# Kernel optimization log

Hardware: AMD Instinct MI355X
Metric: run time of the kernel (lower is better)

## Reference

```python
import jax, jax.numpy as jnp
import numpy as np

N_SRC, N_MID, N_TGT = 200000, 100000, 50000
E1, E2 = 1600000, 800000
D_IN, D_HID, D_OUT = 128, 256, 64


def setup_inputs() -> dict:
    key = jax.random.key(0)
    ks = jax.random.split(key, 10)
    x = jax.random.normal(ks[0], (N_SRC, D_IN), dtype=jnp.float32)
    # edge_index[0] = source node ids, edge_index[1] = target node ids (PyG source_to_target)
    ei1 = jnp.stack([
        jax.random.randint(ks[1], (E1,), 0, N_SRC, dtype=jnp.int32),
        jax.random.randint(ks[2], (E1,), 0, N_MID, dtype=jnp.int32),
    ])
    ei2 = jnp.stack([
        jax.random.randint(ks[3], (E2,), 0, N_MID, dtype=jnp.int32),
        jax.random.randint(ks[4], (E2,), 0, N_TGT, dtype=jnp.int32),
    ])
    s = 1.0 / np.sqrt(D_IN)
    Wl1 = jax.random.uniform(ks[5], (D_IN, D_HID), jnp.float32, -s, s)
    Wr1 = jax.random.uniform(ks[6], (D_IN, D_HID), jnp.float32, -s, s)
    b1 = jnp.zeros((D_HID,), jnp.float32)
    s2 = 1.0 / np.sqrt(D_HID)
    Wl2 = jax.random.uniform(ks[7], (D_HID, D_OUT), jnp.float32, -s2, s2)
    Wr2 = jax.random.uniform(ks[8], (D_HID, D_OUT), jnp.float32, -s2, s2)
    b2 = jnp.zeros((D_OUT,), jnp.float32)
    return {"x": x, "edge_index1": ei1, "edge_index2": ei2,
            "Wl1": Wl1, "Wr1": Wr1, "b1": b1,
            "Wl2": Wl2, "Wr2": Wr2, "b2": b2}


def _sage_conv(x_src, x_tgt, edge_index, Wl, Wr, b, n_tgt):
    # mean aggregation of source features onto targets, then two linear branches
    msg = x_src[edge_index[0]]                                   # [E, d]
    agg = jax.ops.segment_sum(msg, edge_index[1], num_segments=n_tgt)
    cnt = jax.ops.segment_sum(jnp.ones((edge_index.shape[1],), x_src.dtype),
                              edge_index[1], num_segments=n_tgt)
    agg = agg / jnp.maximum(cnt, 1.0)[:, None]
    return agg @ Wl + x_tgt @ Wr + b


def reference(x, edge_index1, edge_index2, Wl1, Wr1, b1, Wl2, Wr2, b2):
    # layer 1: [N_SRC, D_IN] -> [N_MID, D_HID], then ReLU (dropout inactive in eval)
    h = _sage_conv(x, x[:N_MID], edge_index1, Wl1, Wr1, b1, N_MID)
    h = jax.nn.relu(h)
    # layer 2 (final): no activation
    out = _sage_conv(h, h[:N_TGT], edge_index2, Wl2, Wr2, b2, N_TGT)
    return out
```

## Files before the change

### kernel.cpp

```cpp
#include <hip/hip_runtime.h>


#define NSRC 200000
#define NMID 100000
#define NTGT 50000
#define NE1  1600000
#define NE2  800000
#define DIN  128
#define DHID 256
#define DOUT 64

#define XCH (NSRC * 16)

#define CH   4096
#define NBK1 391
#define NBK2 196
#define NCH1 ((NE1 + CH - 1) / CH)
#define NCH2 ((NE2 + CH - 1) / CH)
#define HCH  8192
#define NHC1 ((NE1 + HCH - 1) / HCH)
#define NHC2 ((NE2 + HCH - 1) / HCH)
#define MAXBUF 6144

typedef __attribute__((ext_vector_type(8))) short bf16x8;
typedef __attribute__((ext_vector_type(4))) float f32x4;

__device__ __forceinline__ unsigned short f2bf(float f) {
    unsigned int u = __builtin_bit_cast(unsigned int, f);
    u += 0x7FFFu + ((u >> 16) & 1u);
    return (unsigned short)(u >> 16);
}
__device__ __forceinline__ float bf_lo(unsigned int u) {
    return __builtin_bit_cast(float, u << 16);
}
__device__ __forceinline__ float bf_hi(unsigned int u) {
    return __builtin_bit_cast(float, u & 0xFFFF0000u);
}

__global__ __launch_bounds__(256) void convert_all_kernel(
    const float* __restrict__ x,
    const float* __restrict__ Wl1, const float* __restrict__ Wr1,
    const float* __restrict__ Wl2, const float* __restrict__ Wr2,
    unsigned short* __restrict__ xb, unsigned short* __restrict__ WT1,
    unsigned short* __restrict__ WT2)
{
    int gid = blockIdx.x * 256 + threadIdx.x;
    if (gid < XCH) {
        const float4 v0 = *(const float4*)(x + (long long)gid * 8);
        const float4 v1 = *(const float4*)(x + (long long)gid * 8 + 4);
        unsigned short o[8] = {f2bf(v0.x), f2bf(v0.y), f2bf(v0.z), f2bf(v0.w),
                               f2bf(v1.x), f2bf(v1.y), f2bf(v1.z), f2bf(v1.w)};
        *(uint4*)(xb + (long long)gid * 8) = *(const uint4*)o;
        return;
    }
    int g = gid - XCH;
    if (g < 65536) {
        int n = g >> 8, k = g & 255;
        float v = (k < DIN) ? Wl1[(long long)k * DHID + n]
                            : Wr1[(long long)(k - DIN) * DHID + n];
        WT1[g] = f2bf(v);
        return;
    }
    g -= 65536;
    if (g < 32768) {
        int n2 = g >> 8, k = g & 255;
        float v = (n2 < DOUT) ? Wl2[(long long)k * DOUT + n2]
                              : Wr2[(long long)k * DOUT + (n2 - DOUT)];
        WT2[g] = f2bf(v);
    }
}


__global__ __launch_bounds__(256) void bucket_hist_kernel(
    const int* __restrict__ ei1, const int* __restrict__ ei2,
    int* __restrict__ bhist1, int* __restrict__ bhist2)
{
    __shared__ unsigned int lh[512];
    const int* ei; int* bh; int nE, nbk, chunk;
    if (blockIdx.x < NHC1) { ei = ei1; bh = bhist1; nE = NE1; nbk = NBK1; chunk = blockIdx.x; }
    else { ei = ei2; bh = bhist2; nE = NE2; nbk = NBK2; chunk = blockIdx.x - NHC1; }
    int t = threadIdx.x;
    lh[t] = 0; lh[t + 256] = 0;
    __syncthreads();
    int base = chunk * HCH;
    int end = nE < base + HCH ? nE : base + HCH;
    for (int e = base + t; e < end; e += 256)
        atomicAdd(&lh[((unsigned)ei[nE + e]) >> 8], 1u);
    __syncthreads();
    if (t < nbk && lh[t]) atomicAdd(&bh[t], (int)lh[t]);
    if (t + 256 < nbk && lh[t + 256]) atomicAdd(&bh[t + 256], (int)lh[t + 256]);
}

__global__ __launch_bounds__(256) void bucket_scan_kernel(
    const int* __restrict__ bhist1, const int* __restrict__ bhist2,
    int* __restrict__ bbase1, int* __restrict__ bbase2,
    int* __restrict__ bcur1, int* __restrict__ bcur2,
    int* __restrict__ rs1, int* __restrict__ rs2)
{
    __shared__ int s[256];
    int t = threadIdx.x;
    int a0 = (2 * t < NBK1) ? bhist1[2 * t] : 0;
    int a1 = (2 * t + 1 < NBK1) ? bhist1[2 * t + 1] : 0;
    s[t] = a0 + a1;
    __syncthreads();
    for (int off = 1; off < 256; off <<= 1) {
        int u = (t >= off) ? s[t - off] : 0;
        __syncthreads();
        s[t] += u;
        __syncthreads();
    }
    int ex = (t > 0) ? s[t - 1] : 0;
    if (2 * t < NBK1)     { bbase1[2 * t] = ex;      bcur1[2 * t] = ex; }
    if (2 * t + 1 < NBK1) { bbase1[2 * t + 1] = ex + a0; bcur1[2 * t + 1] = ex + a0; }
    if (t == 0) { bbase1[NBK1] = NE1; rs1[NMID] = NE1; bbase2[NBK2] = NE2; rs2[NTGT] = NE2; }
    __syncthreads();
    int b0 = (t < NBK2) ? bhist2[t] : 0;
    s[t] = b0;
    __syncthreads();
    for (int off = 1; off < 256; off <<= 1) {
        int u = (t >= off) ? s[t - off] : 0;
        __syncthreads();
        s[t] += u;
        __syncthreads();
    }
    int ex2 = (t > 0) ? s[t - 1] : 0;
    if (t < NBK2) { bbase2[t] = ex2; bcur2[t] = ex2; }
}

__global__ __launch_bounds__(256) void bin_kernel(
    const int* __restrict__ ei1, const int* __restrict__ ei2,
    int* __restrict__ bcur1, int* __restrict__ bcur2,
    uint2* __restrict__ gbuf1, uint2* __restrict__ gbuf2)
{
    __shared__ unsigned int lcnt[512];
    __shared__ unsigned int lofs[512];
    __shared__ unsigned int lpos[512];
    __shared__ unsigned int gbase[512];
    __shared__ unsigned int swarp[256];
    __shared__ uint2 lbuf[CH];

    const int* ei; int* bcur; uint2* gbuf; int nE, nbk, chunk;
    if (blockIdx.x < NCH1) {
        ei = ei1; bcur = bcur1; gbuf = gbuf1; nE = NE1; nbk = NBK1; chunk = blockIdx.x;
    } else {
        ei = ei2; bcur = bcur2; gbuf = gbuf2; nE = NE2; nbk = NBK2; chunk = blockIdx.x - NCH1;
    }
    int base = chunk * CH;
    int nb = nE - base; if (nb > CH) nb = CH;
    int t = threadIdx.x;

    for (int i = t; i < 512; i += 256) { lcnt[i] = 0; lpos[i] = 0; }
    __syncthreads();

    int srcv[16], tgtv[16];
    #pragma unroll
    for (int i = 0; i < 16; ++i) {
        int e = base + i * 256 + t;
        if (e < nE) {
            tgtv[i] = ei[nE + e];
            srcv[i] = ei[e];
            atomicAdd(&lcnt[tgtv[i] >> 8], 1u);
        } else tgtv[i] = -1;
    }
    __syncthreads();

    unsigned a0 = lcnt[2 * t], a1 = lcnt[2 * t + 1];
    swarp[t] = a0 + a1;
    __syncthreads();
    for (int off = 1; off < 256; off <<= 1) {
        unsigned v = (t >= off) ? swarp[t - off] : 0;
        __syncthreads();
        swarp[t] += v;
        __syncthreads();
    }
    unsigned ex = (t > 0) ? swarp[t - 1] : 0;
    lofs[2 * t] = ex;
    lofs[2 * t + 1] = ex + a0;
    if (2 * t < nbk && a0) gbase[2 * t] = atomicAdd(&bcur[2 * t], (int)a0);
    if (2 * t + 1 < nbk && a1) gbase[2 * t + 1] = atomicAdd(&bcur[2 * t + 1], (int)a1);
    __syncthreads();

    #pragma unroll
    for (int i = 0; i < 16; ++i) {
        if (tgtv[i] >= 0) {
            int b = tgtv[i] >> 8;
            unsigned idx = lofs[b] + atomicAdd(&lpos[b], 1u);
            lbuf[idx] = make_uint2((unsigned)srcv[i], (unsigned)tgtv[i]);
        }
    }
    __syncthreads();

    for (int i = t; i < nb; i += 256) {
        uint2 r = lbuf[i];
        int b = (int)(r.y >> 8);
        unsigned gi = gbase[b] + ((unsigned)i - lofs[b]);
        gbuf[gi] = r;
    }
}

__global__ __launch_bounds__(256) void bucket_csr_kernel(
    const uint2* __restrict__ gbuf1, const uint2* __restrict__ gbuf2,
    const int* __restrict__ bbase1, const int* __restrict__ bbase2,
    int* __restrict__ rs1, int* __restrict__ rs2,
    int* __restrict__ csr1, int* __restrict__ csr2)
{
    __shared__ unsigned int lhist[256];
    __shared__ unsigned int lcur[256];
    __shared__ unsigned int sscan[256];
    __shared__ unsigned int lbuf[MAXBUF];
    const uint2* gbuf; const int* bbase; int* rs; int* csr; int bucket, ntot;
    if (blockIdx.x < NBK1) {
        gbuf = gbuf1; bbase = bbase1; rs = rs1; csr = csr1; bucket = blockIdx.x; ntot = NMID;
    } else {
        gbuf = gbuf2; bbase = bbase2; rs = rs2; csr = csr2; bucket = blockIdx.x - NBK1; ntot = NTGT;
    }
    int base = bbase[bucket];
    int size = bbase[bucket + 1] - base;
    int node0 = bucket << 8;
    int nnode = ntot - node0; if (nnode > 256) nnode = 256;
    int t = threadIdx.x;
    lhist[t] = 0;
    __syncthreads();
    for (int i = t; i < size; i += 256)
        atomicAdd(&lhist[gbuf[base + i].y & 255], 1u);
    __syncthreads();
    unsigned v = lhist[t];
    sscan[t] = v;
    __syncthreads();
    for (int off = 1; off < 256; off <<= 1) {
        unsigned u = (t >= off) ? sscan[t - off] : 0;
        __syncthreads();
        sscan[t] += u;
        __syncthreads();
    }
    unsigned ex = (t > 0) ? sscan[t - 1] : 0;
    lcur[t] = ex;
    if (t < nnode) rs[node0 + t] = base + (int)ex;
    __syncthreads();
    for (int i = t; i < size; i += 256) {
        uint2 r = gbuf[base + i];
        unsigned pos = atomicAdd(&lcur[r.y & 255], 1u);
        lbuf[pos] = r.x;
    }
    __syncthreads();
    for (int i = t; i < size; i += 256)
        csr[base + i] = (int)lbuf[i];
}


__global__ __launch_bounds__(256) void gather1_kernel(
    const unsigned short* __restrict__ xb, const int* __restrict__ rs,
    const int* __restrict__ csr, unsigned short* __restrict__ aggnb)
{
    int node = blockIdx.x * 4 + (threadIdx.x >> 6);
    if (node >= NMID) return;
    int lane = threadIdx.x & 63;
    int s = rs[node];
    int d = rs[node + 1] - s;
    const char* xbase = (const char*)xb;
    unsigned int voff = (unsigned int)lane * 4u;
    float a0 = 0.f, a1 = 0.f, b0 = 0.f, b1 = 0.f;
    float c0 = 0.f, c1 = 0.f, e0 = 0.f, e1 = 0.f;
    for (int base = 0; base < d; base += 64) {
        int nb = d - base; if (nb > 64) nb = 64;
        int li = base + lane; if (li > d - 1) li = d - 1;
        int my = csr[s + li];
        int j = 0;
        for (; j + 3 < nb; j += 4) {
            int s0 = __builtin_amdgcn_readlane(my, j);
            int s1 = __builtin_amdgcn_readlane(my, j + 1);
            int s2 = __builtin_amdgcn_readlane(my, j + 2);
            int s3 = __builtin_amdgcn_readlane(my, j + 3);
            unsigned int u0 = *(const unsigned int*)(xbase + (((size_t)(unsigned)s0) << 8) + voff);
            unsigned int u1 = *(const unsigned int*)(xbase + (((size_t)(unsigned)s1) << 8) + voff);
            unsigned int u2 = *(const unsigned int*)(xbase + (((size_t)(unsigned)s2) << 8) + voff);
            unsigned int u3 = *(const unsigned int*)(xbase + (((size_t)(unsigned)s3) << 8) + voff);
            a0 += bf_lo(u0); a1 += bf_hi(u0);
            b0 += bf_lo(u1); b1 += bf_hi(u1);
            c0 += bf_lo(u2); c1 += bf_hi(u2);
            e0 += bf_lo(u3); e1 += bf_hi(u3);
        }
        for (; j < nb; ++j) {
            int s0 = __builtin_amdgcn_readlane(my, j);
            unsigned int u0 = *(const unsigned int*)(xbase + (((size_t)(unsigned)s0) << 8) + voff);
            a0 += bf_lo(u0); a1 += bf_hi(u0);
        }
    }
    float inv = (d > 0) ? 1.0f / (float)d : 0.f;
    float r0 = (a0 + b0 + c0 + e0) * inv;
    float r1 = (a1 + b1 + c1 + e1) * inv;
    unsigned int packed = (unsigned int)f2bf(r0) | ((unsigned int)f2bf(r1) << 16);
    *(unsigned int*)(aggnb + (long long)node * DIN + lane * 2) = packed;
}

__global__ __launch_bounds__(256) void gather2_kernel(
    const float* __restrict__ p, const int* __restrict__ rs,
    const int* __restrict__ csr, float* __restrict__ aggp)
{
    int node = blockIdx.x * 4 + (threadIdx.x >> 6);
    if (node >= NTGT) return;
    int lane = threadIdx.x & 63;
    int s = rs[node];
    int d = rs[node + 1] - s;
    const char* pbase = (const char*)p;
    unsigned int voff = (unsigned int)lane * 4u;
    float a = 0.f, b = 0.f, c = 0.f, e = 0.f;
    for (int base = 0; base < d; base += 64) {
        int nb = d - base; if (nb > 64) nb = 64;
        int li = base + lane; if (li > d - 1) li = d - 1;
        int my = csr[s + li];
        int j = 0;
        for (; j + 3 < nb; j += 4) {
            int s0 = __builtin_amdgcn_readlane(my, j);
            int s1 = __builtin_amdgcn_readlane(my, j + 1);
            int s2 = __builtin_amdgcn_readlane(my, j + 2);
            int s3 = __builtin_amdgcn_readlane(my, j + 3);
            a += *(const float*)(pbase + (((size_t)(unsigned)s0) << 8) + voff);
            b += *(const float*)(pbase + (((size_t)(unsigned)s1) << 8) + voff);
            c += *(const float*)(pbase + (((size_t)(unsigned)s2) << 8) + voff);
            e += *(const float*)(pbase + (((size_t)(unsigned)s3) << 8) + voff);
        }
        for (; j < nb; ++j) {
            int s0 = __builtin_amdgcn_readlane(my, j);
            a += *(const float*)(pbase + (((size_t)(unsigned)s0) << 8) + voff);
        }
    }
    float inv = (d > 0) ? 1.0f / (float)d : 0.f;
    aggp[(long long)node * DOUT + lane] = (a + b + c + e) * inv;
}

#define LDSP 40

__global__ __launch_bounds__(256) void gemm1_mfma(
    const unsigned short* __restrict__ aggnb, const unsigned short* __restrict__ xb,
    const unsigned short* __restrict__ WT, const float* __restrict__ bias,
    unsigned short* __restrict__ h)
{
    __shared__ unsigned short Asm[128 * LDSP];
    __shared__ unsigned short Bsm[128 * LDSP];
    const int tid = threadIdx.x;
    const int bm = blockIdx.x * 128;
    const int bn = blockIdx.y * 128;
    const int wave = tid >> 6, lane = tid & 63;
    const int wr = wave >> 1, wc = wave & 1;
    const int lrow = lane & 15, quad = lane >> 4;

    f32x4 acc[4][4];
    #pragma unroll
    for (int i = 0; i < 4; ++i)
        #pragma unroll
        for (int j = 0; j < 4; ++j)
            acc[i][j] = (f32x4){0.f, 0.f, 0.f, 0.f};

    for (int k0 = 0; k0 < 256; k0 += 32) {
        #pragma unroll
        for (int c = tid; c < 512; c += 256) {
            int row = c >> 2, seg = c & 3;
            int grow = bm + row; if (grow >= NMID) grow = NMID - 1;
            int gk = k0 + seg * 8;
            const unsigned short* src = (gk < DIN)
                ? (aggnb + (long long)grow * DIN + gk)
                : (xb + (long long)grow * DIN + (gk - DIN));
            *(uint4*)(Asm + row * LDSP + seg * 8) = *(const uint4*)src;
        }
        #pragma unroll
        for (int c = tid; c < 512; c += 256) {
            int row = c >> 2, seg = c & 3;
            *(uint4*)(Bsm + row * LDSP + seg * 8) =
                *(const uint4*)(WT + (long long)(bn + row) * 256 + k0 + seg * 8);
        }
        __syncthreads();
        bf16x8 af[4], bfr[4];
        #pragma unroll
        for (int mi = 0; mi < 4; ++mi)
            af[mi] = *(const bf16x8*)(Asm + (wr * 64 + mi * 16 + lrow) * LDSP + quad * 8);
        #pragma unroll
        for (int ni = 0; ni < 4; ++ni)
            bfr[ni] = *(const bf16x8*)(Bsm + (wc * 64 + ni * 16 + lrow) * LDSP + quad * 8);
        #pragma unroll
        for (int mi = 0; mi < 4; ++mi)
            #pragma unroll
            for (int ni = 0; ni < 4; ++ni)
                acc[mi][ni] = __builtin_amdgcn_mfma_f32_16x16x32_bf16(
                    af[mi], bfr[ni], acc[mi][ni], 0, 0, 0);
        __syncthreads();
    }
    #pragma unroll
    for (int mi = 0; mi < 4; ++mi) {
        #pragma unroll
        for (int ni = 0; ni < 4; ++ni) {
            int col = bn + wc * 64 + ni * 16 + lrow;
            float bv = bias[col];
            #pragma unroll
            for (int r = 0; r < 4; ++r) {
                int row = bm + wr * 64 + mi * 16 + quad * 4 + r;
                if (row < NMID) {
                    float v = acc[mi][ni][r] + bv;
                    h[(long long)row * DHID + col] = f2bf(fmaxf(v, 0.0f));
                }
            }
        }
    }
}

template <bool FIN>
__global__ __launch_bounds__(256) void gemm_n64_mfma(
    const unsigned short* __restrict__ h, const unsigned short* __restrict__ WT,
    int nofs, int M,
    const float* __restrict__ bias, const float* __restrict__ aggp,
    float* __restrict__ outp)
{
    __shared__ unsigned short Asm[128 * LDSP];
    __shared__ unsigned short Bsm[64 * LDSP];
    const int tid = threadIdx.x;
    const int bm = blockIdx.x * 128;
    const int wave = tid >> 6, lane = tid & 63;
    const int lrow = lane & 15, quad = lane >> 4;

    f32x4 acc[2][4];
    #pragma unroll
    for (int i = 0; i < 2; ++i)
        #pragma unroll
        for (int j = 0; j < 4; ++j)
            acc[i][j] = (f32x4){0.f, 0.f, 0.f, 0.f};

    for (int k0 = 0; k0 < 256; k0 += 32) {
        #pragma unroll
        for (int c = tid; c < 512; c += 256) {
            int row = c >> 2, seg = c & 3;
            int grow = bm + row; if (grow >= M) grow = M - 1;
            *(uint4*)(Asm + row * LDSP + seg * 8) =
                *(const uint4*)(h + (long long)grow * DHID + k0 + seg * 8);
        }
        {
            int row = tid >> 2, seg = tid & 3;
            *(uint4*)(Bsm + row * LDSP + seg * 8) =
                *(const uint4*)(WT + (long long)(nofs + row) * 256 + k0 + seg * 8);
        }
        __syncthreads();
        bf16x8 af[2], bfr[4];
        #pragma unroll
        for (int mi = 0; mi < 2; ++mi)
            af[mi] = *(const bf16x8*)(Asm + (wave * 32 + mi * 16 + lrow) * LDSP + quad * 8);
        #pragma unroll
        for (int ni = 0; ni < 4; ++ni)
            bfr[ni] = *(const bf16x8*)(Bsm + (ni * 16 + lrow) * LDSP + quad * 8);
        #pragma unroll
        for (int mi = 0; mi < 2; ++mi)
            #pragma unroll
            for (int ni = 0; ni < 4; ++ni)
                acc[mi][ni] = __builtin_amdgcn_mfma_f32_16x16x32_bf16(
                    af[mi], bfr[ni], acc[mi][ni], 0, 0, 0);
        __syncthreads();
    }
    #pragma unroll
    for (int mi = 0; mi < 2; ++mi) {
        #pragma unroll
        for (int ni = 0; ni < 4; ++ni) {
            int col = ni * 16 + lrow;
            float bv = FIN ? bias[col] : 0.f;
            #pragma unroll
            for (int r = 0; r < 4; ++r) {
                int row = bm + wave * 32 + mi * 16 + quad * 4 + r;
                if (row < M) {
                    float v = acc[mi][ni][r] + bv;
                    if (FIN) v += aggp[(long long)row * DOUT + col];
                    outp[(long long)row * DOUT + col] = v;
                }
            }
        }
    }
}

extern "C" void kernel_launch(void* const* d_in, const int* in_sizes, int n_in,
                              void* d_out, int out_size, void* d_ws, size_t ws_size,
                              hipStream_t stream) {
    const float* x   = (const float*)d_in[0];
    const int*   ei1 = (const int*)d_in[1];
    const int*   ei2 = (const int*)d_in[2];
    const float* Wl1 = (const float*)d_in[3];
    const float* Wr1 = (const float*)d_in[4];
    const float* b1  = (const float*)d_in[5];
    const float* Wl2 = (const float*)d_in[6];
    const float* Wr2 = (const float*)d_in[7];
    const float* b2  = (const float*)d_in[8];
    float* out = (float*)d_out;

    unsigned short* xb    = (unsigned short*)d_ws;
    unsigned short* aggnb = xb + (size_t)NSRC * DIN;
    unsigned short* h     = aggnb + (size_t)NMID * DIN;
    unsigned short* WT1   = h + (size_t)NMID * DHID;
    unsigned short* WT2   = WT1 + 256 * 256;
    float* p    = (float*)(WT2 + 128 * 256);
    float* aggp = p + (size_t)NMID * DOUT;
    int* rs1    = (int*)(aggp + (size_t)NTGT * DOUT);
    int* rs2    = rs1 + (NMID + 1);
    int* bhist1 = rs2 + (NTGT + 1);
    int* bhist2 = bhist1 + NBK1;
    int* bbase1 = bhist2 + NBK2;
    int* bbase2 = bbase1 + (NBK1 + 1);
    int* bcur1  = bbase2 + (NBK2 + 1);
    int* bcur2  = bcur1 + NBK1;
    int* csr1   = bcur2 + NBK2 + 1;
    int* csr2   = csr1 + NE1;
    uint2* gbuf1 = (uint2*)(((size_t)(csr2 + NE2) + 15) & ~(size_t)15);
    uint2* gbuf2 = gbuf1 + NE1;

    convert_all_kernel<<<(XCH + 65536 + 32768 + 255) / 256, 256, 0, stream>>>(
        x, Wl1, Wr1, Wl2, Wr2, xb, WT1, WT2);

    hipMemsetAsync(bhist1, 0, (size_t)(NBK1 + NBK2) * 4, stream);
    bucket_hist_kernel<<<NHC1 + NHC2, 256, 0, stream>>>(ei1, ei2, bhist1, bhist2);
    bucket_scan_kernel<<<1, 256, 0, stream>>>(bhist1, bhist2, bbase1, bbase2,
                                              bcur1, bcur2, rs1, rs2);
    bin_kernel<<<NCH1 + NCH2, 256, 0, stream>>>(ei1, ei2, bcur1, bcur2, gbuf1, gbuf2);
    bucket_csr_kernel<<<NBK1 + NBK2, 256, 0, stream>>>(
        gbuf1, gbuf2, bbase1, bbase2, rs1, rs2, csr1, csr2);

    gather1_kernel<<<(NMID + 3) / 4, 256, 0, stream>>>(xb, rs1, csr1, aggnb);
    {
        dim3 grid((NMID + 127) / 128, 2);
        gemm1_mfma<<<grid, 256, 0, stream>>>(aggnb, xb, WT1, b1, h);
    }
    gemm_n64_mfma<false><<<(NMID + 127) / 128, 256, 0, stream>>>(
        h, WT2, 0, NMID, nullptr, nullptr, p);
    gather2_kernel<<<(NTGT + 3) / 4, 256, 0, stream>>>(p, rs2, csr2, aggp);
    gemm_n64_mfma<true><<<(NTGT + 127) / 128, 256, 0, stream>>>(
        h, WT2, 64, NTGT, b2, aggp, out);
}
```

Measured before the change: 433.6 us.

## Fuse layer-2 GEMMs into one dual-output pass and prefetch global loads in GEMMs

After: 406.4 us. 6.3% less time.

```diff
diff --git a/kernel.cpp b/kernel.cpp
--- a/kernel.cpp
+++ b/kernel.cpp
@@ -293,9 +293,10 @@
     *(unsigned int*)(aggnb + (long long)node * DIN + lane * 2) = packed;
 }
 
-__global__ __launch_bounds__(256) void gather2_kernel(
-    const float* __restrict__ p, const int* __restrict__ rs,
-    const int* __restrict__ csr, float* __restrict__ aggp)
+__global__ __launch_bounds__(256) void gather2_final_kernel(
+    const float* __restrict__ p, const float* __restrict__ qb,
+    const int* __restrict__ rs, const int* __restrict__ csr,
+    float* __restrict__ out)
 {
     int node = blockIdx.x * 4 + (threadIdx.x >> 6);
     if (node >= NTGT) return;
@@ -326,7 +327,8 @@
         }
     }
     float inv = (d > 0) ? 1.0f / (float)d : 0.f;
-    aggp[(long long)node * DOUT + lane] = (a + b + c + e) * inv;
+    out[(long long)node * DOUT + lane] =
+        qb[(long long)node * DOUT + lane] + (a + b + c + e) * inv;
 }
 
 #define LDSP 40
@@ -345,6 +347,26 @@
     const int wr = wave >> 1, wc = wave & 1;
     const int lrow = lane & 15, quad = lane >> 4;
 
+    const int c0r = tid >> 2, c0s = tid & 3;
+    const int c1r = (tid + 256) >> 2, c1s = tid & 3;
+    int growA0 = bm + c0r; if (growA0 >= NMID) growA0 = NMID - 1;
+    int growA1 = bm + c1r; if (growA1 >= NMID) growA1 = NMID - 1;
+
+    uint4 pa0, pa1, pb0, pb1;
+    auto gload = [&](int k0) {
+        int gk0 = k0 + c0s * 8;
+        const unsigned short* sA0 = (gk0 < DIN)
+            ? (aggnb + (long long)growA0 * DIN + gk0)
+            : (xb + (long long)growA0 * DIN + (gk0 - DIN));
+        pa0 = *(const uint4*)sA0;
+        const unsigned short* sA1 = (gk0 < DIN)
+            ? (aggnb + (long long)growA1 * DIN + gk0)
+            : (xb + (long long)growA1 * DIN + (gk0 - DIN));
+        pa1 = *(const uint4*)sA1;
+        pb0 = *(const uint4*)(WT + (long long)(bn + c0r) * 256 + k0 + c0s * 8);
+        pb1 = *(const uint4*)(WT + (long long)(bn + c1r) * 256 + k0 + c1s * 8);
+    };
+
     f32x4 acc[4][4];
     #pragma unroll
     for (int i = 0; i < 4; ++i)
@@ -352,24 +374,15 @@
         for (int j = 0; j < 4; ++j)
             acc[i][j] = (f32x4){0.f, 0.f, 0.f, 0.f};
 
-    for (int k0 = 0; k0 < 256; k0 += 32) {
-        #pragma unroll
-        for (int c = tid; c < 512; c += 256) {
-            int row = c >> 2, seg = c & 3;
-            int grow = bm + row; if (grow >= NMID) grow = NMID - 1;
-            int gk = k0 + seg * 8;
-            const unsigned short* src = (gk < DIN)
-                ? (aggnb + (long long)grow * DIN + gk)
-                : (xb + (long long)grow * DIN + (gk - DIN));
-            *(uint4*)(Asm + row * LDSP + seg * 8) = *(const uint4*)src;
-        }
-        #pragma unroll
-        for (int c = tid; c < 512; c += 256) {
-            int row = c >> 2, seg = c & 3;
-            *(uint4*)(Bsm + row * LDSP + seg * 8) =
-                *(const uint4*)(WT + (long long)(bn + row) * 256 + k0 + seg * 8);
-        }
-        __syncthreads();
+    gload(0);
+    for (int it = 0; it < 8; ++it) {
+        if (it) __syncthreads();
+        *(uint4*)(Asm + c0r * LDSP + c0s * 8) = pa0;
+        *(uint4*)(Asm + c1r * LDSP + c1s * 8) = pa1;
+        *(uint4*)(Bsm + c0r * LDSP + c0s * 8) = pb0;
+        *(uint4*)(Bsm + c1r * LDSP + c1s * 8) = pb1;
+        __syncthreads();
+        if (it < 7) gload((it + 1) * 32);
         bf16x8 af[4], bfr[4];
         #pragma unroll
         for (int mi = 0; mi < 4; ++mi)
@@ -383,7 +396,6 @@
             for (int ni = 0; ni < 4; ++ni)
                 acc[mi][ni] = __builtin_amdgcn_mfma_f32_16x16x32_bf16(
                     af[mi], bfr[ni], acc[mi][ni], 0, 0, 0);
-        __syncthreads();
     }
     #pragma unroll
     for (int mi = 0; mi < 4; ++mi) {
@@ -403,70 +415,88 @@
     }
 }
 
-template <bool FIN>
-__global__ __launch_bounds__(256) void gemm_n64_mfma(
-    const unsigned short* __restrict__ h, const unsigned short* __restrict__ WT,
-    int nofs, int M,
-    const float* __restrict__ bias, const float* __restrict__ aggp,
-    float* __restrict__ outp)
+__global__ __launch_bounds__(256) void gemm2_dual_mfma(
+    const unsigned short* __restrict__ h, const unsigned short* __restrict__ WT2,
+    const float* __restrict__ b2,
+    float* __restrict__ p, float* __restrict__ qb)
 {
     __shared__ unsigned short Asm[128 * LDSP];
-    __shared__ unsigned short Bsm[64 * LDSP];
+    __shared__ unsigned short Bsm[128 * LDSP];
     const int tid = threadIdx.x;
     const int bm = blockIdx.x * 128;
     const int wave = tid >> 6, lane = tid & 63;
     const int lrow = lane & 15, quad = lane >> 4;
-
-    f32x4 acc[2][4];
+    const bool doq = (bm < NTGT);
+
+    const int c0r = tid >> 2, c0s = tid & 3;
+    const int c1r = (tid + 256) >> 2;
+    int growA0 = bm + c0r; if (growA0 >= NMID) growA0 = NMID - 1;
+    int growA1 = bm + c1r; if (growA1 >= NMID) growA1 = NMID - 1;
+
+    uint4 pa0, pa1, pb0, pb1;
+    auto gload = [&](int k0) {
+        pa0 = *(const uint4*)(h + (long long)growA0 * DHID + k0 + c0s * 8);
+        pa1 = *(const uint4*)(h + (long long)growA1 * DHID + k0 + c0s * 8);
+        pb0 = *(const uint4*)(WT2 + (long long)c0r * 256 + k0 + c0s * 8);
+        pb1 = *(const uint4*)(WT2 + (long long)c1r * 256 + k0 + c0s * 8);
+    };
+
+    f32x4 accP[2][4], accQ[2][4];
     #pragma unroll
     for (int i = 0; i < 2; ++i)
         #pragma unroll
-        for (int j = 0; j < 4; ++j)
-            acc[i][j] = (f32x4){0.f, 0.f, 0.f, 0.f};
-
-    for (int k0 = 0; k0 < 256; k0 += 32) {
-        #pragma unroll
-        for (int c = tid; c < 512; c += 256) {
-            int row = c >> 2, seg = c & 3;
-            int grow = bm + row; if (grow >= M) grow = M - 1;
-            *(uint4*)(Asm + row * LDSP + seg * 8) =
-                *(const uint4*)(h + (long long)grow * DHID + k0 + seg * 8);
-        }
-        {
-            int row = tid >> 2, seg = tid & 3;
-            *(uint4*)(Bsm + row * LDSP + seg * 8) =
-                *(const uint4*)(WT + (long long)(nofs + row) * 256 + k0 + seg * 8);
-        }
-        __syncthreads();
-        bf16x8 af[2], bfr[4];
+        for (int j = 0; j < 4; ++j) {
+            accP[i][j] = (f32x4){0.f, 0.f, 0.f, 0.f};
+            accQ[i][j] = (f32x4){0.f, 0.f, 0.f, 0.f};
+        }
+
+    gload(0);
+    for (int it = 0; it < 8; ++it) {
+        if (it) __syncthreads();
+        *(uint4*)(Asm + c0r * LDSP + c0s * 8) = pa0;
+        *(uint4*)(Asm + c1r * LDSP + c0s * 8) = pa1;
+        *(uint4*)(Bsm + c0r * LDSP + c0s * 8) = pb0;
+        *(uint4*)(Bsm + c1r * LDSP + c0s * 8) = pb1;
+        __syncthreads();
+        if (it < 7) gload((it + 1) * 32);
+        bf16x8 af[2], bp[4];
         #pragma unroll
         for (int mi = 0; mi < 2; ++mi)
             af[mi] = *(const bf16x8*)(Asm + (wave * 32 + mi * 16 + lrow) * LDSP + quad * 8);
         #pragma unroll
         for (int ni = 0; ni < 4; ++ni)
-            bfr[ni] = *(const bf16x8*)(Bsm + (ni * 16 + lrow) * LDSP + quad * 8);
+            bp[ni] = *(const bf16x8*)(Bsm + (ni * 16 + lrow) * LDSP + quad * 8);
         #pragma unroll
         for (int mi = 0; mi < 2; ++mi)
             #pragma unroll
             for (int ni = 0; ni < 4; ++ni)
-                acc[mi][ni] = __builtin_amdgcn_mfma_f32_16x16x32_bf16(
-                    af[mi], bfr[ni], acc[mi][ni], 0, 0, 0);
-        __syncthreads();
+                accP[mi][ni] = __builtin_amdgcn_mfma_f32_16x16x32_bf16(
+                    af[mi], bp[ni], accP[mi][ni], 0, 0, 0);
+        if (doq) {
+            bf16x8 bq[4];
+            #pragma unroll
+            for (int ni = 0; ni < 4; ++ni)
+                bq[ni] = *(const bf16x8*)(Bsm + (64 + ni * 16 + lrow) * LDSP + quad * 8);
+            #pragma unroll
+            for (int mi = 0; mi < 2; ++mi)
+                #pragma unroll
+                for (int ni = 0; ni < 4; ++ni)
+                    accQ[mi][ni] = __builtin_amdgcn_mfma_f32_16x16x32_bf16(
+                        af[mi], bq[ni], accQ[mi][ni], 0, 0, 0);
+        }
     }
     #pragma unroll
     for (int mi = 0; mi < 2; ++mi) {
         #pragma unroll
         for (int ni = 0; ni < 4; ++ni) {
             int col = ni * 16 + lrow;
-            float bv = FIN ? bias[col] : 0.f;
             #pragma unroll
             for (int r = 0; r < 4; ++r) {
                 int row = bm + wave * 32 + mi * 16 + quad * 4 + r;
-                if (row < M) {
-                    float v = acc[mi][ni][r] + bv;
-                    if (FIN) v += aggp[(long long)row * DOUT + col];
-                    outp[(long long)row * DOUT + col] = v;
-                }
+                if (row < NMID)
+                    p[(long long)row * DOUT + col] = accP[mi][ni][r];
+                if (doq && row < NTGT)
+                    qb[(long long)row * DOUT + col] = accQ[mi][ni][r] + b2[col];
             }
         }
     }
@@ -492,8 +522,8 @@
     unsigned short* WT1   = h + (size_t)NMID * DHID;
     unsigned short* WT2   = WT1 + 256 * 256;
     float* p    = (float*)(WT2 + 128 * 256);
-    float* aggp = p + (size_t)NMID * DOUT;
-    int* rs1    = (int*)(aggp + (size_t)NTGT * DOUT);
+    float* qb   = p + (size_t)NMID * DOUT;
+    int* rs1    = (int*)(qb + (size_t)NTGT * DOUT);
     int* rs2    = rs1 + (NMID + 1);
     int* bhist1 = rs2 + (NTGT + 1);
     int* bhist2 = bhist1 + NBK1;
@@ -522,9 +552,6 @@
         dim3 grid((NMID + 127) / 128, 2);
         gemm1_mfma<<<grid, 256, 0, stream>>>(aggnb, xb, WT1, b1, h);
     }
-    gemm_n64_mfma<false><<<(NMID + 127) / 128, 256, 0, stream>>>(
-        h, WT2, 0, NMID, nullptr, nullptr, p);
-    gather2_kernel<<<(NTGT + 3) / 4, 256, 0, stream>>>(p, rs2, csr2, aggp);
-    gemm_n64_mfma<true><<<(NTGT + 127) / 128, 256, 0, stream>>>(
-        h, WT2, 64, NTGT, b2, aggp, out);
-}
+    gemm2_dual_mfma<<<(NMID + 127) / 128, 256, 0, stream>>>(h, WT2, b2, p, qb);
+    gather2_final_kernel<<<(NTGT + 3) / 4, 256, 0, stream>>>(p, qb, rs2, csr2, out);
+}
```
